# Kernel tuning notes

Measured on AMD Instinct MI355X. Metric: run time of the kernel, lower is better.

## Reference

```python
import jax, jax.numpy as jnp
import numpy as np
import math

GROUPS = 32
EPS = 1e-5
NUM_HEADS = 8


def group_norm(x, gamma, beta):
    # x: [B, C, H, W]; normalize within each of GROUPS channel groups over (C/G, H, W)
    B, C, H, W = x.shape
    xg = x.reshape(B, GROUPS, C // GROUPS, H, W)
    mean = jnp.mean(xg, axis=(2, 3, 4), keepdims=True)
    var = jnp.var(xg, axis=(2, 3, 4), keepdims=True)
    xn = ((xg - mean) * jax.lax.rsqrt(var + EPS)).reshape(B, C, H, W)
    return xn * gamma[None, :, None, None] + beta[None, :, None, None]


def setup_inputs() -> dict:
    key = jax.random.key(0)
    ks = jax.random.split(key, 10)
    C = 512
    B, H, W = 2, 64, 64
    s = 1.0 / math.sqrt(C)
    return {
        "x": jax.random.normal(ks[0], (B, C, H, W), jnp.float32),
        "gamma": jnp.ones((C,), jnp.float32),
        "beta": jnp.zeros((C,), jnp.float32),
        "Wq": jax.random.normal(ks[1], (C, C), jnp.float32) * s,
        "bq": jax.random.normal(ks[2], (C,), jnp.float32) * 0.01,
        "Wk": jax.random.normal(ks[3], (C, C), jnp.float32) * s,
        "bk": jax.random.normal(ks[4], (C,), jnp.float32) * 0.01,
        "Wv": jax.random.normal(ks[5], (C, C), jnp.float32) * s,
        "bv": jax.random.normal(ks[6], (C,), jnp.float32) * 0.01,
        "Wo": jax.random.normal(ks[7], (C, C), jnp.float32) * s,
        "bo": jax.random.normal(ks[8], (C,), jnp.float32) * 0.01,
    }


def reference(x, gamma, beta, Wq, bq, Wk, bk, Wv, bv, Wo, bo):
    B, C, H, W = x.shape
    N = H * W
    hd = C // NUM_HEADS
    h = group_norm(x, gamma, beta)
    h = h.reshape(B, C, N).transpose(0, 2, 1)  # [B, N, C]
    # torch nn.Linear: y = x @ W.T + b
    q = (h @ Wq.T + bq).reshape(B, N, NUM_HEADS, hd)
    k = (h @ Wk.T + bk).reshape(B, N, NUM_HEADS, hd)
    v = (h @ Wv.T + bv).reshape(B, N, NUM_HEADS, hd)
    scale = 1.0 / math.sqrt(hd)
    attn = jnp.einsum('bihd,bjhd->bijh', q, k) * scale  # [B, N, N, heads]
    attn = jax.nn.softmax(attn, axis=2)
    o = jnp.einsum('bijh,bjhd->bihd', attn, v).reshape(B, N, C)
    o = o @ Wo.T + bo
    o = o.transpose(0, 2, 1).reshape(B, C, H, W)
    return x + o
```

## Files before the change

kernel.cpp:

```cpp
#include <hip/hip_runtime.h>
#include <cstdint>
#include <cstddef>

typedef __bf16 bf16x8 __attribute__((ext_vector_type(8)));
typedef float f32x4 __attribute__((ext_vector_type(4)));
typedef float f32x16 __attribute__((ext_vector_type(16)));
typedef unsigned short ushort8 __attribute__((ext_vector_type(8)));
typedef float f4 __attribute__((ext_vector_type(4)));

__device__ __forceinline__ unsigned short f2bf(float f) {
    __bf16 b = (__bf16)f;
    return *(unsigned short*)&b;
}
__device__ __forceinline__ unsigned pk2bf(float a, float b) {
    __bf16 x = (__bf16)a, y = (__bf16)b;
    unsigned short ux = *(unsigned short*)&x, uy = *(unsigned short*)&y;
    return (unsigned)ux | ((unsigned)uy << 16);
}

#if __has_builtin(__builtin_amdgcn_exp2f)
#define EXP2(x) __builtin_amdgcn_exp2f(x)
#else
#define EXP2(x) exp2f(x)
#endif

__device__ __forceinline__ void pl32swap(unsigned& x, unsigned& y) {
#if __has_builtin(__builtin_amdgcn_permlane32_swap)
    auto r = __builtin_amdgcn_permlane32_swap(x, y, false, false);
    x = r[0]; y = r[1];
#else
    unsigned xs = (unsigned)__shfl_xor((int)x, 32, 64);
    unsigned ys = (unsigned)__shfl_xor((int)y, 32, 64);
    bool lo = ((threadIdx.x & 63) < 32);
    unsigned nx = lo ? x : ys;
    unsigned ny = lo ? xs : y;
    x = nx; y = ny;
#endif
}

#define GLL(g, l) __builtin_amdgcn_global_load_lds( \
    (__attribute__((address_space(1))) void*)(g), \
    (__attribute__((address_space(3))) void*)(l), 16, 0, 0)

#define CS 0.18033688011112042f

__global__ __launch_bounds__(256) void convert_w(
    const float* __restrict__ wq, const float* __restrict__ wk,
    const float* __restrict__ wv, const float* __restrict__ wo,
    unsigned short* __restrict__ out)
{
    int i = blockIdx.x * 256 + threadIdx.x;
    const float* src = (i < 262144) ? wq : (i < 524288) ? wk : (i < 786432) ? wv : wo;
    out[i] = f2bf(src[i & 262143]);
}

__global__ __launch_bounds__(256) void gn_stats(
    const float* __restrict__ x, float* __restrict__ part)
{
    const int q = blockIdx.x, bg = blockIdx.y;
    const f4* xv = (const f4*)(x + (size_t)bg * 65536 + q * 16384);
    float s = 0.f, sq = 0.f;
    for (int i = threadIdx.x; i < 4096; i += 256) {
        f4 v = xv[i];
        s  += v.x + v.y + v.z + v.w;
        sq += v.x * v.x + v.y * v.y + v.z * v.z + v.w * v.w;
    }
    #pragma unroll
    for (int off = 32; off > 0; off >>= 1) {
        s  += __shfl_xor(s, off, 64);
        sq += __shfl_xor(sq, off, 64);
    }
    __shared__ float red[8];
    const int w = threadIdx.x >> 6, lane = threadIdx.x & 63;
    if (lane == 0) { red[w] = s; red[4 + w] = sq; }
    __syncthreads();
    if (threadIdx.x == 0) {
        part[(bg * 4 + q) * 2]     = red[0] + red[1] + red[2] + red[3];
        part[(bg * 4 + q) * 2 + 1] = red[4] + red[5] + red[6] + red[7];
    }
}

__global__ __launch_bounds__(256) void gn_apply(
    const float* __restrict__ x, const float* __restrict__ gamma,
    const float* __restrict__ beta, const float* __restrict__ part,
    unsigned short* __restrict__ h)
{
    const int q = blockIdx.x, bg = blockIdx.y;
    const int b = bg >> 5, g = bg & 31;
    float s = 0.f, sq = 0.f;
    #pragma unroll
    for (int j = 0; j < 4; ++j) {
        s  += part[(bg * 4 + j) * 2];
        sq += part[(bg * 4 + j) * 2 + 1];
    }
    const float mean = s * (1.f / 65536.f);
    const float rstd = rsqrtf(sq * (1.f / 65536.f) - mean * mean + 1e-5f);

    float gm[16], bt[16];
    #pragma unroll
    for (int c = 0; c < 16; ++c) {
        gm[c] = gamma[g * 16 + c] * rstd;
        bt[c] = beta[g * 16 + c];
    }
    const float* xg = x + (size_t)bg * 65536;
    const int n0 = q * 1024 + threadIdx.x * 4;
    float val[16][4];
    #pragma unroll
    for (int c = 0; c < 16; ++c) {
        f4 v = *(const f4*)&xg[(size_t)c * 4096 + n0];
        val[c][0] = (v.x - mean) * gm[c] + bt[c];
        val[c][1] = (v.y - mean) * gm[c] + bt[c];
        val[c][2] = (v.z - mean) * gm[c] + bt[c];
        val[c][3] = (v.w - mean) * gm[c] + bt[c];
    }
    #pragma unroll
    for (int nn = 0; nn < 4; ++nn) {
        ushort8 v0, v1;
        #pragma unroll
        for (int c = 0; c < 8; ++c)  v0[c]     = f2bf(val[c][nn]);
        #pragma unroll
        for (int c = 8; c < 16; ++c) v1[c - 8] = f2bf(val[c][nn]);
        unsigned short* dst = h + ((size_t)(b * 4096 + n0 + nn)) * 512 + g * 16;
        *(ushort8*)dst = v0;
        *(ushort8*)(dst + 8) = v1;
    }
}

template <int MODE>
__global__ __launch_bounds__(256, 2) void gemm_bt(
    const unsigned short* __restrict__ A,
    const unsigned short* __restrict__ Bt,
    const float* __restrict__ bias0,
    const float* __restrict__ bias1,
    const float* __restrict__ bias2,
    const float* __restrict__ resid,
    void* __restrict__ outp,
    int M, int N, int K)
{
    __shared__ __attribute__((aligned(16))) unsigned short As[128 * 32];
    __shared__ __attribute__((aligned(16))) unsigned short Bs[128 * 32];
    const int t = threadIdx.x;
    const int w = t >> 6, lane = t & 63;
    const int l15 = lane & 15, l4 = lane >> 4;
    const int bm = blockIdx.y, bn = blockIdx.x;
    const int wm = (w >> 1) * 64, wn = (w & 1) * 64;

    f32x4 acc[4][4] = {};

    const int srow = t >> 2;
    const int sc8  = (t & 3) * 8;

    const unsigned short* gA0 = A  + (size_t)(bm * 128 + srow) * K + sc8;
    const unsigned short* gA1 = gA0 + (size_t)64 * K;
    const unsigned short* gB0 = Bt + (size_t)(bn * 128 + srow) * K + sc8;
    const unsigned short* gB1 = gB0 + (size_t)64 * K;
    unsigned short* lA0 = &As[w * 512];
    unsigned short* lA1 = &As[2048 + w * 512];
    unsigned short* lB0 = &Bs[w * 512];
    unsigned short* lB1 = &Bs[2048 + w * 512];

    for (int k0 = 0; k0 < K; k0 += 32) {
        __syncthreads();
        GLL(gA0 + k0, lA0);
        GLL(gA1 + k0, lA1);
        GLL(gB0 + k0, lB0);
        GLL(gB1 + k0, lB1);
        __syncthreads();

        bf16x8 af[4], bfr[4];
        #pragma unroll
        for (int mt = 0; mt < 4; ++mt)
            af[mt] = *(const bf16x8*)&As[(wm + mt * 16 + l15) * 32 + l4 * 8];
        #pragma unroll
        for (int nt = 0; nt < 4; ++nt)
            bfr[nt] = *(const bf16x8*)&Bs[(wn + nt * 16 + l15) * 32 + l4 * 8];
        #pragma unroll
        for (int mt = 0; mt < 4; ++mt)
            #pragma unroll
            for (int nt = 0; nt < 4; ++nt)
                acc[mt][nt] = __builtin_amdgcn_mfma_f32_16x16x32_bf16(
                    af[mt], bfr[nt], acc[mt][nt], 0, 0, 0);
    }

    if (MODE == 0) {
        unsigned short* outB = (unsigned short*)outp;
        #pragma unroll
        for (int nt = 0; nt < 4; ++nt) {
            int col = bn * 128 + wn + nt * 16 + l15;
            const float* bp = (col < 512) ? bias0 : (col < 1024) ? bias1 : bias2;
            float bv = bp[col & 511];
            float sc = (col < 512) ? CS : 1.0f;
            #pragma unroll
            for (int mt = 0; mt < 4; ++mt)
                #pragma unroll
                for (int r = 0; r < 4; ++r) {
                    int row = bm * 128 + wm + mt * 16 + l4 * 4 + r;
                    outB[(size_t)row * N + col] = f2bf((acc[mt][nt][r] + bv) * sc);
                }
        }
    } else {
        float* outF = (float*)outp;
        #pragma unroll
        for (int mt = 0; mt < 4; ++mt)
            #pragma unroll
            for (int nt = 0; nt < 4; ++nt)
                #pragma unroll
                for (int r = 0; r < 4; ++r) {
                    int c = bm * 128 + wm + mt * 16 + l4 * 4 + r;
                    int m = bn * 128 + wn + nt * 16 + l15;
                    int b = m >> 12, n = m & 4095;
                    size_t idx = ((size_t)(b * 512 + c)) * 4096 + n;
                    outF[idx] = acc[mt][nt][r] + bias0[c] + resid[idx];
                }
    }
}

__global__ __launch_bounds__(256) void transpose_v(
    const unsigned short* __restrict__ qkv, unsigned short* __restrict__ vt)
{
    const int bh = blockIdx.y, b = bh >> 3, h = bh & 7;
    const int n0 = blockIdx.x * 64;
    __shared__ __attribute__((aligned(16))) unsigned short tile[64][72];
    const int t = threadIdx.x;
    #pragma unroll
    for (int j = 0; j < 2; ++j) {
        int chunk = j * 256 + t;
        int nl = chunk >> 3, d8 = (chunk & 7) * 8;
        *(ushort8*)&tile[nl][d8] =
            *(const ushort8*)(qkv + ((size_t)(b * 4096 + n0 + nl)) * 1536 + 1024 + h * 64 + d8);
    }
    __syncthreads();
    #pragma unroll
    for (int j = 0; j < 2; ++j) {
        int chunk = j * 256 + t;
        int d = chunk >> 3, n8 = (chunk & 7) * 8;
        ushort8 val;
        #pragma unroll
        for (int i = 0; i < 8; ++i) val[i] = tile[n8 + i][d];
        *(ushort8*)(vt + ((size_t)(bh * 64 + d)) * 4096 + n0 + n8) = val;
    }
}

__global__ __launch_bounds__(128, 1) void attn_kernel(
    const unsigned short* __restrict__ qkv, const unsigned short* __restrict__ vt,
    unsigned short* __restrict__ o)
{
    __shared__ __attribute__((aligned(16))) unsigned short Ks[64][72];
    __shared__ __attribute__((aligned(16))) unsigned short Vts[64][72];
    __shared__ __attribute__((aligned(16))) unsigned short Oepi[128][72];

    const int bh = blockIdx.y, b = bh >> 3, h = bh & 7;
    const int row0 = blockIdx.x * 128;
    const int t = threadIdx.x, w = t >> 6, lane = t & 63;
    const int l31 = lane & 31, h5 = lane >> 5;

    const unsigned short* Qg = qkv + ((size_t)(b * 4096 + row0 + w * 64)) * 1536 + h * 64;
    const unsigned short* Kg = qkv + ((size_t)(b * 4096)) * 1536 + 512 + h * 64;
    const unsigned short* Vg = vt + ((size_t)bh) * 64 * 4096;

    bf16x8 qf[2][4];
    #pragma unroll
    for (int qt = 0; qt < 2; ++qt)
        #pragma unroll
        for (int kc = 0; kc < 4; ++kc)
            qf[qt][kc] = *(const bf16x8*)(Qg + (size_t)(qt * 32 + l31) * 1536 + kc * 16 + h5 * 8);

    f32x16 Oacc[2][2] = {};
    float li[2] = {0.f, 0.f};

    const int sr = t >> 1, sc0 = (t & 1) * 32;
    const unsigned short* gK = Kg + (size_t)sr * 1536 + sc0;
    const unsigned short* gV = Vg + (size_t)sr * 4096 + sc0;
    unsigned short* lK = &Ks[sr][sc0];
    unsigned short* lV = &Vts[sr][sc0];

    ushort8 kr[4], vr[4];
    #pragma unroll
    for (int j = 0; j < 4; ++j) {
        kr[j] = *(const ushort8*)(gK + j * 8);
        vr[j] = *(const ushort8*)(gV + j * 8);
    }

    for (int kt = 0; kt < 64; ++kt) {
        __syncthreads();
        #pragma unroll
        for (int j = 0; j < 4; ++j) {
            *(ushort8*)(lK + j * 8) = kr[j];
            *(ushort8*)(lV + j * 8) = vr[j];
        }
        __syncthreads();
        if (kt < 63) {
            const unsigned short* nk = gK + (size_t)(kt + 1) * 64 * 1536;
            const unsigned short* nv = gV + (kt + 1) * 64;
            #pragma unroll
            for (int j = 0; j < 4; ++j) {
                kr[j] = *(const ushort8*)(nk + j * 8);
                vr[j] = *(const ushort8*)(nv + j * 8);
            }
        }

        f32x16 St[2][2] = {};
        #pragma unroll
        for (int ct = 0; ct < 2; ++ct)
            #pragma unroll
            for (int kc = 0; kc < 4; ++kc) {
                bf16x8 kf = *(const bf16x8*)&Ks[ct * 32 + l31][kc * 16 + h5 * 8];
                St[0][ct] = __builtin_amdgcn_mfma_f32_32x32x16_bf16(kf, qf[0][kc], St[0][ct], 0, 0, 0);
                St[1][ct] = __builtin_amdgcn_mfma_f32_32x32x16_bf16(kf, qf[1][kc], St[1][ct], 0, 0, 0);
            }

        union PU { unsigned u[4]; bf16x8 v; };
        PU pf[2][4];
        #pragma unroll
        for (int qt = 0; qt < 2; ++qt) {
            #pragma unroll
            for (int ct = 0; ct < 2; ++ct)
                #pragma unroll
                for (int r = 0; r < 16; ++r)
                    St[qt][ct][r] = EXP2(St[qt][ct][r]);
            float s0 = 0.f, s1 = 0.f;
            #pragma unroll
            for (int ct = 0; ct < 2; ++ct) {
                s0 += ((St[qt][ct][0] + St[qt][ct][1]) + (St[qt][ct][2] + St[qt][ct][3]))
                    + ((St[qt][ct][4] + St[qt][ct][5]) + (St[qt][ct][6] + St[qt][ct][7]));
                s1 += ((St[qt][ct][8] + St[qt][ct][9]) + (St[qt][ct][10] + St[qt][ct][11]))
                    + ((St[qt][ct][12] + St[qt][ct][13]) + (St[qt][ct][14] + St[qt][ct][15]));
            }
            li[qt] += s0 + s1;

            #pragma unroll
            for (int ct = 0; ct < 2; ++ct) {
                unsigned pk0 = pk2bf(St[qt][ct][0],  St[qt][ct][1]);
                unsigned pk1 = pk2bf(St[qt][ct][2],  St[qt][ct][3]);
                unsigned pk2 = pk2bf(St[qt][ct][4],  St[qt][ct][5]);
                unsigned pk3 = pk2bf(St[qt][ct][6],  St[qt][ct][7]);
                unsigned pk4 = pk2bf(St[qt][ct][8],  St[qt][ct][9]);
                unsigned pk5 = pk2bf(St[qt][ct][10], St[qt][ct][11]);
                unsigned pk6 = pk2bf(St[qt][ct][12], St[qt][ct][13]);
                unsigned pk7 = pk2bf(St[qt][ct][14], St[qt][ct][15]);
                pl32swap(pk0, pk2); pl32swap(pk1, pk3);
                pl32swap(pk4, pk6); pl32swap(pk5, pk7);
                pf[qt][ct * 2].u[0] = pk0; pf[qt][ct * 2].u[1] = pk1;
                pf[qt][ct * 2].u[2] = pk2; pf[qt][ct * 2].u[3] = pk3;
                pf[qt][ct * 2 + 1].u[0] = pk4; pf[qt][ct * 2 + 1].u[1] = pk5;
                pf[qt][ct * 2 + 1].u[2] = pk6; pf[qt][ct * 2 + 1].u[3] = pk7;
            }
        }

        #pragma unroll
        for (int kk = 0; kk < 4; ++kk)
            #pragma unroll
            for (int dt = 0; dt < 2; ++dt) {
                bf16x8 vf = *(const bf16x8*)&Vts[dt * 32 + l31][kk * 16 + h5 * 8];
                Oacc[dt][0] = __builtin_amdgcn_mfma_f32_32x32x16_bf16(vf, pf[0][kk].v, Oacc[dt][0], 0, 0, 0);
                Oacc[dt][1] = __builtin_amdgcn_mfma_f32_32x32x16_bf16(vf, pf[1][kk].v, Oacc[dt][1], 0, 0, 0);
            }
    }

    #pragma unroll
    for (int qt = 0; qt < 2; ++qt) {
        float lf = li[qt] + __shfl_xor(li[qt], 32, 64);
        float inv = 1.f / lf;
        #pragma unroll
        for (int dt = 0; dt < 2; ++dt)
            #pragma unroll
            for (int p = 0; p < 8; ++p) {
                int d = dt * 32 + 2 * (p & 1) + 8 * (p >> 1) + 4 * h5;
                unsigned u = pk2bf(Oacc[dt][qt][2 * p] * inv, Oacc[dt][qt][2 * p + 1] * inv);
                *(unsigned*)&Oepi[w * 64 + qt * 32 + l31][d] = u;
            }
    }
    unsigned short* Og = o + ((size_t)(b * 4096 + row0 + w * 64)) * 512 + h * 64;
    #pragma unroll
    for (int c8 = 0; c8 < 8; ++c8) {
        ushort8 val = *(const ushort8*)&Oepi[w * 64 + lane][c8 * 8];
        *(ushort8*)(Og + (size_t)lane * 512 + c8 * 8) = val;
    }
}

extern "C" void kernel_launch(void* const* d_in, const int* in_sizes, int n_in,
                              void* d_out, int out_size, void* d_ws, size_t ws_size,
                              hipStream_t stream) {
    const float* x     = (const float*)d_in[0];
    const float* gamma = (const float*)d_in[1];
    const float* beta  = (const float*)d_in[2];
    const float* Wq    = (const float*)d_in[3];
    const float* bq    = (const float*)d_in[4];
    const float* Wk    = (const float*)d_in[5];
    const float* bk    = (const float*)d_in[6];
    const float* Wv    = (const float*)d_in[7];
    const float* bv    = (const float*)d_in[8];
    const float* Wo    = (const float*)d_in[9];
    const float* bo    = (const float*)d_in[10];
    float* out = (float*)d_out;

    char* ws = (char*)d_ws;
    const size_t MB = 1024 * 1024;
    unsigned short* h      = (unsigned short*)(ws);
    unsigned short* qkv    = (unsigned short*)(ws + 8 * MB);
    unsigned short* vtb    = (unsigned short*)(ws + 32 * MB);
    unsigned short* wb     = (unsigned short*)(ws + 40 * MB);
    float*          gnpart = (float*)(ws + 42 * MB);

    convert_w<<<dim3(4096), dim3(256), 0, stream>>>(Wq, Wk, Wv, Wo, wb);
    gn_stats<<<dim3(4, 64), dim3(256), 0, stream>>>(x, gnpart);
    gn_apply<<<dim3(4, 64), dim3(256), 0, stream>>>(x, gamma, beta, gnpart, h);

    gemm_bt<0><<<dim3(12, 64), dim3(256), 0, stream>>>(
        h, wb, bq, bk, bv, nullptr, qkv, 8192, 1536, 512);

    transpose_v<<<dim3(64, 16), dim3(256), 0, stream>>>(qkv, vtb);

    attn_kernel<<<dim3(32, 16), dim3(128), 0, stream>>>(qkv, vtb, h);

    gemm_bt<1><<<dim3(64, 4), dim3(256), 0, stream>>>(
        wb + 786432, h, bo, nullptr, nullptr, x, out, 512, 8192, 512);
}
```

Before: 235.0 us.

## Split attention over key halves with combine pass, fuse V transpose into QKV GEMM

The QKV GEMM epilogue now writes V directly in transposed per-head layout, so the separate transpose kernel is gone. Attention now uses 256-thread blocks covering 256 queries and a split of the key range into two halves (grid z=2). Each half writes an unnormalized bf16 partial output plus its softmax row sums, and a new combine kernel adds the partials and normalizes. This raises the number of resident waves on the GPU at the cost of an extra partial-output round trip through memory. The combine assumes both splits share the same running max or none is used, and the partials are rounded to bf16 before being summed.

```diff
diff --git a/kernel.cpp b/kernel.cpp
--- a/kernel.cpp
+++ b/kernel.cpp
@@ -6,6 +6,7 @@
 typedef float f32x4 __attribute__((ext_vector_type(4)));
 typedef float f32x16 __attribute__((ext_vector_type(16)));
 typedef unsigned short ushort8 __attribute__((ext_vector_type(8)));
+typedef unsigned u32x2 __attribute__((ext_vector_type(2)));
 typedef float f4 __attribute__((ext_vector_type(4)));
 
 __device__ __forceinline__ unsigned short f2bf(float f) {
@@ -16,6 +17,9 @@
     __bf16 x = (__bf16)a, y = (__bf16)b;
     unsigned short ux = *(unsigned short*)&x, uy = *(unsigned short*)&y;
     return (unsigned)ux | ((unsigned)uy << 16);
+}
+__device__ __forceinline__ float bf2f(unsigned short u) {
+    union { unsigned u; float f; } v; v.u = ((unsigned)u) << 16; return v.f;
 }
 
 #if __has_builtin(__builtin_amdgcn_exp2f)
@@ -135,6 +139,7 @@
     const float* __restrict__ bias2,
     const float* __restrict__ resid,
     void* __restrict__ outp,
+    unsigned short* __restrict__ vtout,
     int M, int N, int K)
 {
     __shared__ __attribute__((aligned(16))) unsigned short As[128 * 32];
@@ -189,14 +194,30 @@
             int col = bn * 128 + wn + nt * 16 + l15;
             const float* bp = (col < 512) ? bias0 : (col < 1024) ? bias1 : bias2;
             float bv = bp[col & 511];
-            float sc = (col < 512) ? CS : 1.0f;
-            #pragma unroll
-            for (int mt = 0; mt < 4; ++mt)
+            if (col < 1024) {
+                float sc = (col < 512) ? CS : 1.0f;
                 #pragma unroll
-                for (int r = 0; r < 4; ++r) {
-                    int row = bm * 128 + wm + mt * 16 + l4 * 4 + r;
-                    outB[(size_t)row * N + col] = f2bf((acc[mt][nt][r] + bv) * sc);
+                for (int mt = 0; mt < 4; ++mt)
+                    #pragma unroll
+                    for (int r = 0; r < 4; ++r) {
+                        int row = bm * 128 + wm + mt * 16 + l4 * 4 + r;
+                        outB[(size_t)row * N + col] = f2bf((acc[mt][nt][r] + bv));
+                        if (col < 512)
+                            outB[(size_t)row * N + col] = f2bf((acc[mt][nt][r] + bv) * CS);
+                    }
+            } else {
+                int hd = col - 1024;
+                #pragma unroll
+                for (int mt = 0; mt < 4; ++mt) {
+                    int m = bm * 128 + wm + mt * 16 + l4 * 4;
+                    int bb = m >> 12, n = m & 4095;
+                    unsigned u0 = pk2bf(acc[mt][nt][0] + bv, acc[mt][nt][1] + bv);
+                    unsigned u1 = pk2bf(acc[mt][nt][2] + bv, acc[mt][nt][3] + bv);
+                    unsigned short* dst = vtout +
+                        ((size_t)(bb * 8 + (hd >> 6)) * 64 + (hd & 63)) * 4096 + n;
+                    *(u32x2*)dst = (u32x2){u0, u1};
                 }
+            }
         }
     } else {
         float* outF = (float*)outp;
@@ -215,48 +236,23 @@
     }
 }
 
-__global__ __launch_bounds__(256) void transpose_v(
-    const unsigned short* __restrict__ qkv, unsigned short* __restrict__ vt)
-{
-    const int bh = blockIdx.y, b = bh >> 3, h = bh & 7;
-    const int n0 = blockIdx.x * 64;
-    __shared__ __attribute__((aligned(16))) unsigned short tile[64][72];
-    const int t = threadIdx.x;
-    #pragma unroll
-    for (int j = 0; j < 2; ++j) {
-        int chunk = j * 256 + t;
-        int nl = chunk >> 3, d8 = (chunk & 7) * 8;
-        *(ushort8*)&tile[nl][d8] =
-            *(const ushort8*)(qkv + ((size_t)(b * 4096 + n0 + nl)) * 1536 + 1024 + h * 64 + d8);
-    }
-    __syncthreads();
-    #pragma unroll
-    for (int j = 0; j < 2; ++j) {
-        int chunk = j * 256 + t;
-        int d = chunk >> 3, n8 = (chunk & 7) * 8;
-        ushort8 val;
-        #pragma unroll
-        for (int i = 0; i < 8; ++i) val[i] = tile[n8 + i][d];
-        *(ushort8*)(vt + ((size_t)(bh * 64 + d)) * 4096 + n0 + n8) = val;
-    }
-}
-
-__global__ __launch_bounds__(128, 1) void attn_kernel(
+__global__ __launch_bounds__(256, 2) void attn_kernel(
     const unsigned short* __restrict__ qkv, const unsigned short* __restrict__ vt,
-    unsigned short* __restrict__ o)
+    unsigned short* __restrict__ opart, float* __restrict__ lbuf)
 {
     __shared__ __attribute__((aligned(16))) unsigned short Ks[64][72];
     __shared__ __attribute__((aligned(16))) unsigned short Vts[64][72];
-    __shared__ __attribute__((aligned(16))) unsigned short Oepi[128][72];
+    __shared__ __attribute__((aligned(16))) unsigned short Oepi[256][72];
 
     const int bh = blockIdx.y, b = bh >> 3, h = bh & 7;
-    const int row0 = blockIdx.x * 128;
+    const int qbase = blockIdx.x * 256;
+    const int s = blockIdx.z, ks0 = s * 2048;
     const int t = threadIdx.x, w = t >> 6, lane = t & 63;
     const int l31 = lane & 31, h5 = lane >> 5;
 
-    const unsigned short* Qg = qkv + ((size_t)(b * 4096 + row0 + w * 64)) * 1536 + h * 64;
-    const unsigned short* Kg = qkv + ((size_t)(b * 4096)) * 1536 + 512 + h * 64;
-    const unsigned short* Vg = vt + ((size_t)bh) * 64 * 4096;
+    const unsigned short* Qg = qkv + ((size_t)(b * 4096 + qbase + w * 64)) * 1536 + h * 64;
+    const unsigned short* Kg = qkv + ((size_t)(b * 4096 + ks0)) * 1536 + 512 + h * 64;
+    const unsigned short* Vg = vt + ((size_t)bh) * 64 * 4096 + ks0;
 
     bf16x8 qf[2][4];
     #pragma unroll
@@ -268,35 +264,32 @@
     f32x16 Oacc[2][2] = {};
     float li[2] = {0.f, 0.f};
 
-    const int sr = t >> 1, sc0 = (t & 1) * 32;
-    const unsigned short* gK = Kg + (size_t)sr * 1536 + sc0;
-    const unsigned short* gV = Vg + (size_t)sr * 4096 + sc0;
-    unsigned short* lK = &Ks[sr][sc0];
-    unsigned short* lV = &Vts[sr][sc0];
-
-    ushort8 kr[4], vr[4];
-    #pragma unroll
-    for (int j = 0; j < 4; ++j) {
-        kr[j] = *(const ushort8*)(gK + j * 8);
-        vr[j] = *(const ushort8*)(gV + j * 8);
-    }
-
-    for (int kt = 0; kt < 64; ++kt) {
+    const int sr = t >> 2, sc = (t & 3) * 16;
+    const unsigned short* gK = Kg + (size_t)sr * 1536 + sc;
+    const unsigned short* gV = Vg + (size_t)sr * 4096 + sc;
+    unsigned short* lK = &Ks[sr][sc];
+    unsigned short* lV = &Vts[sr][sc];
+
+    ushort8 kr[2], vr[2];
+    kr[0] = *(const ushort8*)(gK);
+    kr[1] = *(const ushort8*)(gK + 8);
+    vr[0] = *(const ushort8*)(gV);
+    vr[1] = *(const ushort8*)(gV + 8);
+
+    for (int kt = 0; kt < 32; ++kt) {
         __syncthreads();
-        #pragma unroll
-        for (int j = 0; j < 4; ++j) {
-            *(ushort8*)(lK + j * 8) = kr[j];
-            *(ushort8*)(lV + j * 8) = vr[j];
-        }
+        *(ushort8*)(lK)     = kr[0];
+        *(ushort8*)(lK + 8) = kr[1];
+        *(ushort8*)(lV)     = vr[0];
+        *(ushort8*)(lV + 8) = vr[1];
         __syncthreads();
-        if (kt < 63) {
+        if (kt < 31) {
             const unsigned short* nk = gK + (size_t)(kt + 1) * 64 * 1536;
             const unsigned short* nv = gV + (kt + 1) * 64;
-            #pragma unroll
-            for (int j = 0; j < 4; ++j) {
-                kr[j] = *(const ushort8*)(nk + j * 8);
-                vr[j] = *(const ushort8*)(nv + j * 8);
-            }
+            kr[0] = *(const ushort8*)(nk);
+            kr[1] = *(const ushort8*)(nk + 8);
+            vr[0] = *(const ushort8*)(nv);
+            vr[1] = *(const ushort8*)(nv + 8);
         }
 
         f32x16 St[2][2] = {};
@@ -360,22 +353,41 @@
     #pragma unroll
     for (int qt = 0; qt < 2; ++qt) {
         float lf = li[qt] + __shfl_xor(li[qt], 32, 64);
-        float inv = 1.f / lf;
+        if (h5 == 0)
+            lbuf[((size_t)s * 16 + bh) * 4096 + qbase + w * 64 + qt * 32 + l31] = lf;
         #pragma unroll
         for (int dt = 0; dt < 2; ++dt)
             #pragma unroll
             for (int p = 0; p < 8; ++p) {
                 int d = dt * 32 + 2 * (p & 1) + 8 * (p >> 1) + 4 * h5;
-                unsigned u = pk2bf(Oacc[dt][qt][2 * p] * inv, Oacc[dt][qt][2 * p + 1] * inv);
+                unsigned u = pk2bf(Oacc[dt][qt][2 * p], Oacc[dt][qt][2 * p + 1]);
                 *(unsigned*)&Oepi[w * 64 + qt * 32 + l31][d] = u;
             }
     }
-    unsigned short* Og = o + ((size_t)(b * 4096 + row0 + w * 64)) * 512 + h * 64;
+    unsigned short* Og = opart + (((size_t)s * 16 + bh) * 4096 + qbase + w * 64) * 64;
     #pragma unroll
     for (int c8 = 0; c8 < 8; ++c8) {
         ushort8 val = *(const ushort8*)&Oepi[w * 64 + lane][c8 * 8];
-        *(ushort8*)(Og + (size_t)lane * 512 + c8 * 8) = val;
-    }
+        *(ushort8*)(Og + (size_t)lane * 64 + c8 * 8) = val;
+    }
+}
+
+__global__ __launch_bounds__(256) void combine_o(
+    const unsigned short* __restrict__ opart, const float* __restrict__ lbuf,
+    unsigned short* __restrict__ o)
+{
+    int gid = blockIdx.x * 256 + threadIdx.x;
+    int row = gid >> 3, c8 = gid & 7;
+    int bh = row >> 12, q = row & 4095;
+    int b = bh >> 3, h = bh & 7;
+    float inv = 1.f / (lbuf[row] + lbuf[65536 + row]);
+    ushort8 o0 = *(const ushort8*)(opart + (size_t)row * 64 + c8 * 8);
+    ushort8 o1 = *(const ushort8*)(opart + (size_t)65536 * 64 + (size_t)row * 64 + c8 * 8);
+    ushort8 r;
+    #pragma unroll
+    for (int i = 0; i < 8; ++i)
+        r[i] = f2bf((bf2f(o0[i]) + bf2f(o1[i])) * inv);
+    *(ushort8*)(o + ((size_t)(b * 4096 + q)) * 512 + h * 64 + c8 * 8) = r;
 }
 
 extern "C" void kernel_launch(void* const* d_in, const int* in_sizes, int n_in,
@@ -401,18 +413,19 @@
     unsigned short* vtb    = (unsigned short*)(ws + 32 * MB);
     unsigned short* wb     = (unsigned short*)(ws + 40 * MB);
     float*          gnpart = (float*)(ws + 42 * MB);
+    unsigned short* opart  = (unsigned short*)(ws + 43 * MB);
+    float*          lbuf   = (float*)(ws + 59 * MB);
 
     convert_w<<<dim3(4096), dim3(256), 0, stream>>>(Wq, Wk, Wv, Wo, wb);
     gn_stats<<<dim3(4, 64), dim3(256), 0, stream>>>(x, gnpart);
     gn_apply<<<dim3(4, 64), dim3(256), 0, stream>>>(x, gamma, beta, gnpart, h);
 
     gemm_bt<0><<<dim3(12, 64), dim3(256), 0, stream>>>(
-        h, wb, bq, bk, bv, nullptr, qkv, 8192, 1536, 512);
-
-    transpose_v<<<dim3(64, 16), dim3(256), 0, stream>>>(qkv, vtb);
-
-    attn_kernel<<<dim3(32, 16), dim3(128), 0, stream>>>(qkv, vtb, h);
+        h, wb, bq, bk, bv, nullptr, qkv, vtb, 8192, 1536, 512);
+
+    attn_kernel<<<dim3(16, 16, 2), dim3(256), 0, stream>>>(qkv, vtb, opart, lbuf);
+    combine_o<<<dim3(2048), dim3(256), 0, stream>>>(opart, lbuf, h);
 
     gemm_bt<1><<<dim3(64, 4), dim3(256), 0, stream>>>(
-        wb + 786432, h, bo, nullptr, nullptr, x, out, 512, 8192, 512);
-}
+        wb + 786432, h, bo, nullptr, nullptr, x, out, nullptr, 512, 8192, 512);
+}
```

After: 221.4 us. 5.8% less time.
